# Optimization experiments

Hardware: AMD Instinct MI355X
Metric: run time of the kernel (lower is better)

## Reference

```python
import jax, jax.numpy as jnp
import numpy as np

S = 8        # parallel streams (encoder/decoder pairs)
T_ENC = 12   # encoder timesteps per stream
H = 256      # hidden size
F = 316      # input features
B = 1024     # batch
MAX_LEN = 48
SCALE = 1.0 / np.sqrt(H).astype(np.float32)  # MHA single-head scaling


def _lstm_gates_to_hc(gates, c):
    # PyTorch gate order: i, f, g, o
    i, f, g, o = jnp.split(gates, 4, axis=-1)
    c_new = jax.nn.sigmoid(f) * c + jax.nn.sigmoid(i) * jnp.tanh(g)
    h_new = jax.nn.sigmoid(o) * jnp.tanh(c_new)
    return h_new, c_new


def setup_inputs() -> dict:
    key = jax.random.key(0)
    ks = jax.random.split(key, 20)
    w = 0.05
    inp = {
        'x': jax.random.normal(ks[0], (B, 96, F), jnp.float32),
        'tgt': jax.random.normal(ks[1], (B, MAX_LEN), jnp.float32),
        # encoder LSTM (per-stream stacked): input F -> H
        'W_ih_e': jax.random.normal(ks[2], (S, 4 * H, F), jnp.float32) * w,
        'W_hh_e': jax.random.normal(ks[3], (S, 4 * H, H), jnp.float32) * w,
        'b_ih_e': jnp.zeros((S, 4 * H), jnp.float32),
        'b_hh_e': jnp.zeros((S, 4 * H), jnp.float32),
        # decoder LSTM: input 1 -> H
        'W_ih_d': jax.random.normal(ks[4], (S, 4 * H, 1), jnp.float32) * w,
        'W_hh_d': jax.random.normal(ks[5], (S, 4 * H, H), jnp.float32) * w,
        'b_ih_d': jnp.zeros((S, 4 * H), jnp.float32),
        'b_hh_d': jnp.zeros((S, 4 * H), jnp.float32),
        # MultiheadAttention: in_proj [3H,H] per stream, out_proj [H,H]
        'W_in_attn': jax.random.normal(ks[6], (S, 3 * H, H), jnp.float32) * w,
        'b_in_attn': jnp.zeros((S, 3 * H), jnp.float32),
        'W_out_attn': jax.random.normal(ks[7], (S, H, H), jnp.float32) * w,
        'b_out_attn': jnp.zeros((S, H), jnp.float32),
        # decoder out_fc: 2H -> 1
        'W_fcout': jax.random.normal(ks[8], (S, 1, 2 * H), jnp.float32) * w,
        'b_fcout': jnp.zeros((S, 1), jnp.float32),
        # final fc: 8 -> 1
        'W_fc': jax.random.normal(ks[9], (1, S), jnp.float32) * w,
        'b_fc': jnp.zeros((1,), jnp.float32),
    }
    return inp


def _forward(x, tgt, W_ih_e, W_hh_e, b_ih_e, b_hh_e,
             W_ih_d, W_hh_d, b_ih_d, b_hh_d,
             W_in_attn, b_in_attn, W_out_attn, b_out_attn,
             W_fcout, b_fcout, W_fc, b_fc):
    batch, max_len = x.shape[0], tgt.shape[1]
    # time-major then split 96 steps into 8 streams of 12: [S, T_ENC, B, F]
    xe = x.transpose(1, 0, 2).reshape(S, T_ENC, batch, F)

    # ---- encoders: batched LSTM over 8 streams ----
    def enc_step(carry, xt):  # xt [S,B,F]
        h, c = carry
        gates = (jnp.einsum('sbf,sgf->sbg', xt, W_ih_e) + b_ih_e[:, None, :]
                 + jnp.einsum('sbh,sgh->sbg', h, W_hh_e) + b_hh_e[:, None, :])
        h, c = _lstm_gates_to_hc(gates, c)
        return (h, c), h

    h0 = jnp.zeros((S, batch, H), x.dtype)
    (hT, cT), enc_out = jax.lax.scan(enc_step, (h0, h0), xe.transpose(1, 0, 2, 3))
    # enc_out: [T_ENC, S, B, H]; (hT, cT) seed the decoder hidden state

    # ---- precompute attention K,V ----
    Wq, Wk, Wv = jnp.split(W_in_attn, 3, axis=1)  # each [S,H,H]
    bq, bk, bv = jnp.split(b_in_attn, 3, axis=1)  # each [S,H]
    k = jnp.einsum('tsbh,seh->tsbe', enc_out, Wk) + bk[None, :, None, :]
    v = jnp.einsum('tsbh,seh->tsbe', enc_out, Wv) + bv[None, :, None, :]

    # teacher-forced decoder inputs: step 0 uses x[-1,:,0], step t uses tgt[:,t-1]
    inputs = jnp.concatenate([x[:, -1, 0][None, :], tgt.T[:-1]], axis=0)  # [L,B]

    def dec_step(carry, inp):  # inp [B]
        h, c = carry
        it = jnp.broadcast_to(inp[None, :, None], (S, h.shape[1], 1))
        gates = (jnp.einsum('sbi,sgi->sbg', it, W_ih_d) + b_ih_d[:, None, :]
                 + jnp.einsum('sbh,sgh->sbg', h, W_hh_d) + b_hh_d[:, None, :])
        h, c = _lstm_gates_to_hc(gates, c)
        # single-query MHA (1 head) against encoder outputs
        q = jnp.einsum('sbh,seh->sbe', h, Wq) + bq[:, None, :]
        scores = jnp.einsum('sbe,tsbe->sbt', q, k) * SCALE
        attn = jax.nn.softmax(scores, axis=-1)
        ctx = jnp.einsum('sbt,tsbe->sbe', attn, v)
        ctx = jnp.einsum('sbe,soe->sbo', ctx, W_out_attn) + b_out_attn[:, None, :]
        cat = jnp.concatenate([h, ctx], axis=-1)  # [S,B,2H]
        out = jnp.einsum('sbk,sok->sbo', cat, W_fcout) + b_fcout[:, None, :]
        return (h, c), out[..., 0]  # [S,B]

    _, outs = jax.lax.scan(dec_step, (hT, cT), inputs)  # [L,S,B]
    final = outs.transpose(0, 2, 1)                      # [L,B,S]
    y = jnp.einsum('lbs,os->lbo', final, W_fc) + b_fc    # [L,B,1]
    return y[..., 0].T                                    # [B,L]


def reference(x, tgt, W_ih_e, W_hh_e, b_ih_e, b_hh_e,
              W_ih_d, W_hh_d, b_ih_d, b_hh_d,
              W_in_attn, b_in_attn, W_out_attn, b_out_attn,
              W_fcout, b_fcout, W_fc, b_fc):
    return _forward(x, tgt, W_ih_e, W_hh_e, b_ih_e, b_hh_e,
                    W_ih_d, W_hh_d, b_ih_d, b_hh_d,
                    W_in_attn, b_in_attn, W_out_attn, b_out_attn,
                    W_fcout, b_fcout, W_fc, b_fc)
```

## Files before the change

kernel.cpp:

```cpp
#include <hip/hip_runtime.h>
#include <cstdio>
#include <cstdint>

#define S8     8
#define TENC   12
#define HDIM   256
#define FDIM   316
#define BATCH  1024
#define LDEC   48
#define DBT    32
#define KA     264
#define SCALE_ATTN 0.0625f

typedef short bf16x8 __attribute__((ext_vector_type(8)));
typedef float f32x4  __attribute__((ext_vector_type(4)));

__device__ __forceinline__ float sigf(float x) { return 1.0f / (1.0f + expf(-x)); }

__device__ __forceinline__ unsigned short f2bf(float f) {
  unsigned u = __builtin_bit_cast(unsigned, f);
  unsigned r = (u + 0x7fffu + ((u >> 16) & 1u)) >> 16;
  return (unsigned short)r;
}
__device__ __forceinline__ float bflo(unsigned u) {
  return __builtin_bit_cast(float, u << 16);
}
__device__ __forceinline__ float bfhi(unsigned u) {
  return __builtin_bit_cast(float, u & 0xffff0000u);
}

#define MFMA(acc, a, b) acc = __builtin_amdgcn_mfma_f32_16x16x32_bf16(a, b, acc, 0, 0, 0)

#define DOT8(a, q, hp) \
  a = fmaf(bflo(q.x), hp[0], a); a = fmaf(bfhi(q.x), hp[1], a); \
  a = fmaf(bflo(q.y), hp[2], a); a = fmaf(bfhi(q.y), hp[3], a); \
  a = fmaf(bflo(q.z), hp[4], a); a = fmaf(bfhi(q.z), hp[5], a); \
  a = fmaf(bflo(q.w), hp[6], a); a = fmaf(bfhi(q.w), hp[7], a);

#define UNPS(dst, off, q) \
  dst[off+0] = bflo(q.x); dst[off+1] = bfhi(q.x); \
  dst[off+2] = bflo(q.y); dst[off+3] = bfhi(q.y); \
  dst[off+4] = bflo(q.z); dst[off+5] = bfhi(q.z); \
  dst[off+6] = bflo(q.w); dst[off+7] = bfhi(q.w);

__global__ __launch_bounds__(256) void transpose_k(const float* __restrict__ in,
                                                   float* __restrict__ out,
                                                   int R, int C) {
  __shared__ float tile[32][33];
  const int s = blockIdx.z;
  const size_t base = (size_t)s * R * C;
  const int r0 = blockIdx.y * 32, c0 = blockIdx.x * 32;
  const int tx = threadIdx.x & 31, ty = threadIdx.x >> 5;
  for (int i = ty; i < 32; i += 8) {
    int r = r0 + i, c = c0 + tx;
    if (r < R && c < C) tile[i][tx] = in[base + (size_t)r * C + c];
  }
  __syncthreads();
  for (int i = ty; i < 32; i += 8) {
    int c = c0 + i, r = r0 + tx;
    if (c < C && r < R) out[base + (size_t)c * R + r] = tile[tx][i];
  }
}

__global__ __launch_bounds__(256) void fold_gemm(const float* __restrict__ A, size_t sA,
                                                 const float* __restrict__ Bm, size_t sB,
                                                 float* __restrict__ out, size_t sO) {
  const int s = blockIdx.y, r0 = blockIdx.x * 32, col = threadIdx.x;
  A += (size_t)s * sA; Bm += (size_t)s * sB; out += (size_t)s * sO;
  float acc[32] = {};
  for (int e = 0; e < HDIM; ++e) {
    const float bvv = Bm[(size_t)e * HDIM + col];
#pragma unroll
    for (int r = 0; r < 32; ++r) acc[r] = fmaf(A[(size_t)e * HDIM + r0 + r], bvv, acc[r]);
  }
  for (int r = 0; r < 32; ++r) out[(size_t)(r0 + r) * HDIM + col] = acc[r];
}

__global__ __launch_bounds__(64) void pack_hl(const float* __restrict__ src, int Ksrc, int ksT,
                                              bf16x8* __restrict__ outhi,
                                              bf16x8* __restrict__ outlo) {
  const int s = blockIdx.z, ks = blockIdx.y, nt = blockIdx.x;
  const int lane = threadIdx.x, l15 = lane & 15, quad = lane >> 4;
  const int n = nt * 16 + l15, kb = ks * 32 + quad * 8;
  const float* row = src + ((size_t)s * 1024 + n) * Ksrc;
  union { bf16x8 v; unsigned short e[8]; } h, l;
#pragma unroll
  for (int j = 0; j < 8; ++j) {
    const int k = kb + j;
    const float v = (k < Ksrc) ? row[k] : 0.f;
    const unsigned short hi = f2bf(v);
    h.e[j] = hi;
    l.e[j] = f2bf(v - bflo(hi));
  }
  const size_t idx = (((size_t)s * ksT + ks) * 64 + nt) * 64 + lane;
  outhi[idx] = h.v;
  outlo[idx] = l.v;
}

__global__ __launch_bounds__(64) void pack_s(const float* __restrict__ src, int ntOff,
                                             bf16x8* __restrict__ out) {
  const int s = blockIdx.z, ks = blockIdx.y, nt = blockIdx.x;
  const int lane = threadIdx.x, l15 = lane & 15, quad = lane >> 4;
  const int n = nt * 16 + l15, kb = ks * 32 + quad * 8;
  const float* row = src + ((size_t)s * 256 + n) * 256;
  union { bf16x8 v; unsigned short e[8]; } h;
#pragma unroll
  for (int j = 0; j < 8; ++j) h.e[j] = f2bf(row[kb + j]);
  out[(((size_t)s * 8 + ks) * 32 + ntOff + nt) * 64 + lane] = h.v;
}

__global__ __launch_bounds__(256) void fold_vec2(const float* __restrict__ Win,
                                                 const float* __restrict__ bin,
                                                 const float* __restrict__ Wout,
                                                 const float* __restrict__ bout,
                                                 float* __restrict__ kbv,
                                                 float* __restrict__ cbias) {
  const int s = blockIdx.x, t = threadIdx.x;
  const float* bq = bin + s * 768;
  const float* bv = bin + s * 768 + 512;
  float a0 = 0.f, a1 = 0.f;
  for (int e = 0; e < 256; ++e) {
    a0 = fmaf(Win[((size_t)s * 768 + 256 + e) * 256 + t], bq[e], a0);
    a1 = fmaf(Wout[((size_t)s * 256 + t) * 256 + e], bv[e], a1);
  }
  kbv[s * 256 + t] = a0;
  cbias[s * 256 + t] = a1 + bout[s * 256 + t];
}

__global__ __launch_bounds__(256) void fold_mvw(const float* __restrict__ Mv,
                                                const float* __restrict__ Wfo,
                                                float* __restrict__ mvw) {
  const int s = blockIdx.x, k = threadIdx.x;
  float a = 0.f;
  for (int o = 0; o < 256; ++o)
    a = fmaf(Wfo[s * 512 + 256 + o], Mv[((size_t)s * 256 + o) * 256 + k], a);
  mvw[s * 256 + k] = a;
}

__global__ void fold_bias(const float* __restrict__ a, const float* __restrict__ b,
                          float* __restrict__ o, int n) {
  int i = blockIdx.x * 256 + threadIdx.x;
  if (i < n) o[i] = a[i] + b[i];
}

__global__ void build_decin(const float* __restrict__ x, const float* __restrict__ tgt,
                            float* __restrict__ dec_in) {
  int idx = blockIdx.x * 256 + threadIdx.x;
  if (idx >= LDEC * BATCH) return;
  int l = idx >> 10, b = idx & 1023;
  dec_in[idx] = (l == 0) ? x[(size_t)b * 96 * FDIM + 95 * FDIM]
                         : tgt[(size_t)b * LDEC + (l - 1)];
}

__global__ __launch_bounds__(512) void rec_phase(
    const float* __restrict__ x,
    const bf16x8* __restrict__ WxH, const bf16x8* __restrict__ WxL,
    const bf16x8* __restrict__ WeH, const bf16x8* __restrict__ WeL,
    const bf16x8* __restrict__ WdH, const bf16x8* __restrict__ WdL,
    const float* __restrict__ be, const float* __restrict__ bd,
    const float* __restrict__ wihd, const float* __restrict__ Wfo,
    const float* __restrict__ decin,
    unsigned* __restrict__ hEnc,
    unsigned short* __restrict__ hDec,
    float* __restrict__ hdPart)
{
  __shared__ unsigned short hAhi[DBT * KA];
  __shared__ unsigned short hAlo[DBT * KA];
  __shared__ float scrR[DBT * 8];

  const int bid = blockIdx.x;
  const int s = bid & 7, b0 = (bid >> 3) * DBT;
  const int tid = threadIdx.x;
  const int w = tid >> 6, lane = tid & 63, l15 = lane & 15, quad = lane >> 4;

  for (int i = tid; i < DBT * KA; i += 512) { hAhi[i] = 0; hAlo[i] = 0; }

  float beV[4][2], bdV[4][2], wdV[4][2], wfoV[2];
#pragma unroll
  for (int g = 0; g < 4; ++g)
#pragma unroll
    for (int st = 0; st < 2; ++st) {
      const int J = g * 256 + 32 * w + 16 * st + l15;
      beV[g][st] = be[s * 1024 + J];
      bdV[g][st] = bd[s * 1024 + J];
      wdV[g][st] = wihd[s * 1024 + J];
    }
#pragma unroll
  for (int st = 0; st < 2; ++st) wfoV[st] = Wfo[s * 512 + 32 * w + 16 * st + l15];

  float cst[2][2][4];
#pragma unroll
  for (int a = 0; a < 2; ++a)
#pragma unroll
    for (int b = 0; b < 2; ++b)
#pragma unroll
      for (int r = 0; r < 4; ++r) cst[a][b][r] = 0.f;

  const bf16x8* wxh = WxH + (size_t)s * 10 * 64 * 64;
  const bf16x8* wxl = WxL + (size_t)s * 10 * 64 * 64;
  const bf16x8* weh = WeH + (size_t)s * 8 * 64 * 64;
  const bf16x8* wel = WeL + (size_t)s * 8 * 64 * 64;
  const bf16x8* wdh = WdH + (size_t)s * 8 * 64 * 64;
  const bf16x8* wdl = WdL + (size_t)s * 8 * 64 * 64;

  __syncthreads();

  for (int t = 0; t < TENC; ++t) {
    f32x4 acc[2][2][4];
#pragma unroll
    for (int mt = 0; mt < 2; ++mt)
#pragma unroll
      for (int st = 0; st < 2; ++st)
#pragma unroll
        for (int c = 0; c < 4; ++c) acc[mt][st][c] = (f32x4){0.f, 0.f, 0.f, 0.f};

    const size_t xoff = (size_t)(s * TENC + t) * FDIM;
    for (int ks = 0; ks < 10; ++ks) {
      bf16x8 axh[2], axl[2];
#pragma unroll
      for (int mt = 0; mt < 2; ++mt) {
        const f32x4* xr = (const f32x4*)(x + (size_t)(b0 + 16 * mt + l15) * (96 * FDIM)
                                         + xoff + ks * 32 + quad * 8);
        const f32x4 v0 = __builtin_nontemporal_load(xr);
        f32x4 v1;
        if (ks == 9 && quad == 3) v1 = (f32x4){0.f, 0.f, 0.f, 0.f};
        else v1 = __builtin_nontemporal_load(xr + 1);
        float vv[8];
#pragma unroll
        for (int j = 0; j < 4; ++j) { vv[j] = v0[j]; vv[4 + j] = v1[j]; }
        union { bf16x8 v; unsigned short e[8]; } uh, ul;
#pragma unroll
        for (int j = 0; j < 8; ++j) {
          const unsigned short hi = f2bf(vv[j]);
          uh.e[j] = hi;
          ul.e[j] = f2bf(vv[j] - bflo(hi));
        }
        axh[mt] = uh.v; axl[mt] = ul.v;
      }
#pragma unroll
      for (int st = 0; st < 2; ++st)
#pragma unroll
        for (int c = 0; c < 4; ++c) {
          const int nt = c * 16 + 2 * w + st;
          const bf16x8 bh = wxh[(ks * 64 + nt) * 64 + lane];
          const bf16x8 bl = wxl[(ks * 64 + nt) * 64 + lane];
          MFMA(acc[0][st][c], axh[0], bh); MFMA(acc[0][st][c], axh[0], bl); MFMA(acc[0][st][c], axl[0], bh);
          MFMA(acc[1][st][c], axh[1], bh); MFMA(acc[1][st][c], axh[1], bl); MFMA(acc[1][st][c], axl[1], bh);
        }
    }
#pragma unroll 2
    for (int ks = 0; ks < 8; ++ks) {
      bf16x8 ah[2], al[2];
#pragma unroll
      for (int mt = 0; mt < 2; ++mt) {
        const int ao = (16 * mt + l15) * KA + ks * 32 + quad * 8;
        ah[mt] = *(const bf16x8*)&hAhi[ao];
        al[mt] = *(const bf16x8*)&hAlo[ao];
      }
#pragma unroll
      for (int st = 0; st < 2; ++st)
#pragma unroll
        for (int c = 0; c < 4; ++c) {
          const int nt = c * 16 + 2 * w + st;
          const bf16x8 bh = weh[(ks * 64 + nt) * 64 + lane];
          const bf16x8 bl = wel[(ks * 64 + nt) * 64 + lane];
          MFMA(acc[0][st][c], ah[0], bh); MFMA(acc[0][st][c], ah[0], bl); MFMA(acc[0][st][c], al[0], bh);
          MFMA(acc[1][st][c], ah[1], bh); MFMA(acc[1][st][c], ah[1], bl); MFMA(acc[1][st][c], al[1], bh);
        }
    }
    float hv[2][2][4];
#pragma unroll
    for (int mt = 0; mt < 2; ++mt)
#pragma unroll
      for (int st = 0; st < 2; ++st)
#pragma unroll
        for (int reg = 0; reg < 4; ++reg) {
          const float gi = sigf(acc[mt][st][0][reg] + beV[0][st]);
          const float gf = sigf(acc[mt][st][1][reg] + beV[1][st]);
          const float gg = tanhf(acc[mt][st][2][reg] + beV[2][st]);
          const float go = sigf(acc[mt][st][3][reg] + beV[3][st]);
          const float cn = fmaf(gf, cst[mt][st][reg], gi * gg);
          cst[mt][st][reg] = cn;
          hv[mt][st][reg] = go * tanhf(cn);
        }
    __syncthreads();
#pragma unroll
    for (int mt = 0; mt < 2; ++mt)
#pragma unroll
      for (int st = 0; st < 2; ++st)
#pragma unroll
        for (int reg = 0; reg < 4; ++reg) {
          const int R = 16 * mt + 4 * quad + reg;
          const int J = 32 * w + 16 * st + l15;
          const float v = hv[mt][st][reg];
          const unsigned short hi = f2bf(v);
          const unsigned short lo = f2bf(v - bflo(hi));
          hAhi[R * KA + J] = hi;
          hAlo[R * KA + J] = lo;
          __builtin_nontemporal_store((unsigned)hi | ((unsigned)lo << 16),
              &hEnc[((size_t)(t * S8 + s) * BATCH + b0 + R) * HDIM + J]);
        }
    __syncthreads();
  }

  for (int l = 0; l < LDEC; ++l) {
    f32x4 acc[2][2][4];
#pragma unroll
    for (int mt = 0; mt < 2; ++mt)
#pragma unroll
      for (int st = 0; st < 2; ++st)
#pragma unroll
        for (int c = 0; c < 4; ++c) acc[mt][st][c] = (f32x4){0.f, 0.f, 0.f, 0.f};

#pragma unroll 2
    for (int ks = 0; ks < 8; ++ks) {
      bf16x8 ah[2], al[2];
#pragma unroll
      for (int mt = 0; mt < 2; ++mt) {
        const int ao = (16 * mt + l15) * KA + ks * 32 + quad * 8;
        ah[mt] = *(const bf16x8*)&hAhi[ao];
        al[mt] = *(const bf16x8*)&hAlo[ao];
      }
#pragma unroll
      for (int st = 0; st < 2; ++st)
#pragma unroll
        for (int c = 0; c < 4; ++c) {
          const int nt = c * 16 + 2 * w + st;
          const bf16x8 bh = wdh[(ks * 64 + nt) * 64 + lane];
          const bf16x8 bl = wdl[(ks * 64 + nt) * 64 + lane];
          MFMA(acc[0][st][c], ah[0], bh); MFMA(acc[0][st][c], ah[0], bl); MFMA(acc[0][st][c], al[0], bh);
          MFMA(acc[1][st][c], ah[1], bh); MFMA(acc[1][st][c], ah[1], bl); MFMA(acc[1][st][c], al[1], bh);
        }
    }
    float hv[2][2][4];
#pragma unroll
    for (int mt = 0; mt < 2; ++mt)
#pragma unroll
      for (int reg = 0; reg < 4; ++reg) {
        const int R = 16 * mt + 4 * quad + reg;
        const float it = decin[(size_t)l * BATCH + b0 + R];
#pragma unroll
        for (int st = 0; st < 2; ++st) {
          const float gi = sigf(fmaf(it, wdV[0][st], acc[mt][st][0][reg] + bdV[0][st]));
          const float gf = sigf(fmaf(it, wdV[1][st], acc[mt][st][1][reg] + bdV[1][st]));
          const float gg = tanhf(fmaf(it, wdV[2][st], acc[mt][st][2][reg] + bdV[2][st]));
          const float go = sigf(fmaf(it, wdV[3][st], acc[mt][st][3][reg] + bdV[3][st]));
          const float cn = fmaf(gf, cst[mt][st][reg], gi * gg);
          cst[mt][st][reg] = cn;
          hv[mt][st][reg] = go * tanhf(cn);
        }
      }
    __syncthreads();
#pragma unroll
    for (int mt = 0; mt < 2; ++mt)
#pragma unroll
      for (int st = 0; st < 2; ++st)
#pragma unroll
        for (int reg = 0; reg < 4; ++reg) {
          const int R = 16 * mt + 4 * quad + reg;
          const int J = 32 * w + 16 * st + l15;
          const float v = hv[mt][st][reg];
          const unsigned short hi = f2bf(v);
          hAhi[R * KA + J] = hi;
          hAlo[R * KA + J] = f2bf(v - bflo(hi));
          __builtin_nontemporal_store(hi,
              &hDec[((size_t)(l * S8 + s) * BATCH + b0 + R) * HDIM + J]);
        }
    {
      float part[8];
#pragma unroll
      for (int mt = 0; mt < 2; ++mt)
#pragma unroll
        for (int reg = 0; reg < 4; ++reg)
          part[mt * 4 + reg] = hv[mt][0][reg] * wfoV[0] + hv[mt][1][reg] * wfoV[1];
#pragma unroll
      for (int i = 0; i < 8; ++i) {
        float v = part[i];
        v += __shfl_xor(v, 1, 16);
        v += __shfl_xor(v, 2, 16);
        v += __shfl_xor(v, 4, 16);
        v += __shfl_xor(v, 8, 16);
        part[i] = v;
      }
      if (l15 == 0) {
#pragma unroll
        for (int mt = 0; mt < 2; ++mt)
#pragma unroll
          for (int reg = 0; reg < 4; ++reg)
            scrR[(16 * mt + 4 * quad + reg) * 8 + w] = part[mt * 4 + reg];
      }
    }
    __syncthreads();
    if (tid < DBT) {
      float a = 0.f;
#pragma unroll
      for (int p = 0; p < 8; ++p) a += scrR[tid * 8 + p];
      hdPart[((size_t)l * S8 + s) * BATCH + b0 + tid] = a;
    }
  }
}

__global__ __launch_bounds__(256) void attn_phase(
    const unsigned* __restrict__ hEnc, const unsigned short* __restrict__ hDec,
    const bf16x8* __restrict__ AMvF,
    const float* __restrict__ kbv, const float* __restrict__ cbias,
    const float* __restrict__ mvw,
    const float* __restrict__ Wfo, const float* __restrict__ bfo,
    const float* __restrict__ hdPart,
    float* __restrict__ douts)
{
  __shared__ unsigned short kpL[TENC][16][KA];
  __shared__ float scr[16 * TENC * 17];
  __shared__ float sc[16][TENC];
  __shared__ float kbs[TENC][16];
  __shared__ float vw[TENC][16];

  const int s = blockIdx.y, b0 = blockIdx.x * 16;
  const int tid = threadIdx.x;
  const int w = tid >> 6, lane = tid & 63, l15 = lane & 15, quad = lane >> 4;

  const bf16x8* amv = AMvF + (size_t)s * 8 * 32 * 64;
  const float* kvv = kbv + s * 256;
  const float* mvv = mvw + s * 256;
  const float* cbs = cbias + s * 256;
  const float* wfo = Wfo + s * 512;
  const float bfos = bfo[s];

  float cw = 0.f;
  for (int e = 0; e < 256; ++e) cw = fmaf(cbs[e], wfo[256 + e], cw);

  for (int t = 0; t < TENC; ++t) {
    f32x4 acc[4];
#pragma unroll
    for (int c = 0; c < 4; ++c) acc[c] = (f32x4){0.f, 0.f, 0.f, 0.f};
    for (int ks = 0; ks < 8; ++ks) {
      const unsigned* hp = hEnc + ((size_t)(t * S8 + s) * BATCH + b0 + l15) * HDIM
                         + ks * 32 + quad * 8;
      union { bf16x8 v; unsigned short e[8]; } uh, ul;
#pragma unroll
      for (int j = 0; j < 8; ++j) {
        const unsigned u = hp[j];
        uh.e[j] = (unsigned short)u;
        ul.e[j] = (unsigned short)(u >> 16);
      }
#pragma unroll
      for (int c = 0; c < 4; ++c) {
        const int nt = w * 4 + c;
        const bf16x8 b = amv[(ks * 32 + nt) * 64 + lane];
        MFMA(acc[c], uh.v, b); MFMA(acc[c], ul.v, b);
// ... 84 lines not shown
#pragma unroll
  for (int s = 0; s < S8; ++s)
    a = fmaf(douts[((size_t)l * S8 + s) * BATCH + b], Wfc[s], a);
  out[idx] = a;
}

extern "C" void kernel_launch(void* const* d_in, const int* in_sizes, int n_in,
                              void* d_out, int out_size, void* d_ws, size_t ws_size,
                              hipStream_t stream) {
  const float* x          = (const float*)d_in[0];
  const float* tgt        = (const float*)d_in[1];
  const float* W_ih_e     = (const float*)d_in[2];
  const float* W_hh_e     = (const float*)d_in[3];
  const float* b_ih_e     = (const float*)d_in[4];
  const float* b_hh_e     = (const float*)d_in[5];
  const float* W_ih_d     = (const float*)d_in[6];
  const float* W_hh_d     = (const float*)d_in[7];
  const float* b_ih_d     = (const float*)d_in[8];
  const float* b_hh_d     = (const float*)d_in[9];
  const float* W_in_attn  = (const float*)d_in[10];
  const float* b_in_attn  = (const float*)d_in[11];
  const float* W_out_attn = (const float*)d_in[12];
  const float* b_out_attn = (const float*)d_in[13];
  const float* W_fcout    = (const float*)d_in[14];
  const float* b_fcout    = (const float*)d_in[15];
  const float* W_fc       = (const float*)d_in[16];
  const float* b_fc       = (const float*)d_in[17];

  char* wsb = (char*)d_ws;
  size_t off = 0;
  auto alloc = [&](size_t bytes) {
    void* p = wsb + off; off += (bytes + 255) & ~(size_t)255; return p;
  };
  float*  douts = (float*)alloc((size_t)LDEC * S8 * BATCH * 4);
  float*  decin = (float*)alloc((size_t)LDEC * BATCH * 4);
  float*  hdPart= (float*)alloc((size_t)LDEC * S8 * BATCH * 4);
  float*  Pmat  = (float*)alloc((size_t)S8 * 256 * 256 * 4);
  float*  Mvmat = (float*)alloc((size_t)S8 * 256 * 256 * 4);
  float*  WoT   = (float*)alloc((size_t)S8 * 256 * 256 * 4);
  bf16x8* WxH   = (bf16x8*)alloc((size_t)S8 * 10 * 64 * 64 * 16);
  bf16x8* WxL   = (bf16x8*)alloc((size_t)S8 * 10 * 64 * 64 * 16);
  bf16x8* WeH   = (bf16x8*)alloc((size_t)S8 * 8 * 64 * 64 * 16);
  bf16x8* WeL   = (bf16x8*)alloc((size_t)S8 * 8 * 64 * 64 * 16);
  bf16x8* WdH   = (bf16x8*)alloc((size_t)S8 * 8 * 64 * 64 * 16);
  bf16x8* WdL   = (bf16x8*)alloc((size_t)S8 * 8 * 64 * 64 * 16);
  bf16x8* AMvF  = (bf16x8*)alloc((size_t)S8 * 8 * 32 * 64 * 16);
  float*  kbv   = (float*)alloc((size_t)S8 * 256 * 4);
  float*  cbias = (float*)alloc((size_t)S8 * 256 * 4);
  float*  mvw   = (float*)alloc((size_t)S8 * 256 * 4);
  float*  beF   = (float*)alloc((size_t)S8 * 1024 * 4);
  float*  bdF   = (float*)alloc((size_t)S8 * 1024 * 4);
  unsigned* hEnc = (unsigned*)alloc((size_t)TENC * S8 * BATCH * HDIM * 4);
  unsigned short* hDec = (unsigned short*)alloc((size_t)LDEC * S8 * BATCH * HDIM * 2);
  if (off > ws_size) {
    fprintf(stderr, "kernel_launch: ws too small: need %zu bytes, have %zu\n", off, ws_size);
    return;
  }

  transpose_k<<<dim3(8, 8, S8), 256, 0, stream>>>(W_out_attn, WoT, 256, 256);
  fold_gemm<<<dim3(8, S8), 256, 0, stream>>>(W_in_attn, (size_t)768 * 256,
                                             W_in_attn + 256 * 256, (size_t)768 * 256,
                                             Pmat, (size_t)256 * 256);
  fold_gemm<<<dim3(8, S8), 256, 0, stream>>>(WoT, (size_t)256 * 256,
                                             W_in_attn + 2 * 256 * 256, (size_t)768 * 256,
                                             Mvmat, (size_t)256 * 256);
  pack_hl<<<dim3(64, 10, S8), 64, 0, stream>>>(W_ih_e, FDIM, 10, WxH, WxL);
  pack_hl<<<dim3(64, 8, S8), 64, 0, stream>>>(W_hh_e, 256, 8, WeH, WeL);
  pack_hl<<<dim3(64, 8, S8), 64, 0, stream>>>(W_hh_d, 256, 8, WdH, WdL);
  pack_s<<<dim3(16, 8, S8), 64, 0, stream>>>(Pmat, 0, AMvF);
  fold_vec2<<<S8, 256, 0, stream>>>(W_in_attn, b_in_attn, W_out_attn, b_out_attn, kbv, cbias);
  fold_mvw<<<S8, 256, 0, stream>>>(Mvmat, W_fcout, mvw);
  fold_bias<<<(S8 * 1024 + 255) / 256, 256, 0, stream>>>(b_ih_e, b_hh_e, beF, S8 * 1024);
  fold_bias<<<(S8 * 1024 + 255) / 256, 256, 0, stream>>>(b_ih_d, b_hh_d, bdF, S8 * 1024);
  build_decin<<<(LDEC * BATCH + 255) / 256, 256, 0, stream>>>(x, tgt, decin);

  rec_phase<<<256, 512, 0, stream>>>(
      x, WxH, WxL, WeH, WeL, WdH, WdL, beF, bdF, W_ih_d, W_fcout, decin,
      hEnc, hDec, hdPart);

  attn_phase<<<dim3(64, S8), 256, 0, stream>>>(
      hEnc, hDec, AMvF, kbv, cbias, mvw, W_fcout, b_fcout, hdPart, douts);

  final_fc<<<(BATCH * LDEC + 255) / 256, 256, 0, stream>>>(douts, W_fc, b_fc, (float*)d_out);
}
```

Before: 3.228 ms.

## Halve recurrent batch tile to 16 rows and use 512 blocks of 4 waves

```diff
diff --git a/kernel.cpp b/kernel.cpp
--- a/kernel.cpp
+++ b/kernel.cpp
@@ -8,7 +8,7 @@
 #define FDIM   316
 #define BATCH  1024
 #define LDEC   48
-#define DBT    32
+#define DBT    16
 #define KA     264
 #define SCALE_ATTN 0.0625f
 
@@ -152,7 +152,7 @@
                          : tgt[(size_t)b * LDEC + (l - 1)];
 }
 
-__global__ __launch_bounds__(512) void rec_phase(
+__global__ __launch_bounds__(256) void rec_phase(
     const float* __restrict__ x,
     const bf16x8* __restrict__ WxH, const bf16x8* __restrict__ WxL,
     const bf16x8* __restrict__ WeH, const bf16x8* __restrict__ WeL,
@@ -166,35 +166,33 @@
 {
   __shared__ unsigned short hAhi[DBT * KA];
   __shared__ unsigned short hAlo[DBT * KA];
-  __shared__ float scrR[DBT * 8];
+  __shared__ float scrR[DBT * 4];
 
   const int bid = blockIdx.x;
   const int s = bid & 7, b0 = (bid >> 3) * DBT;
   const int tid = threadIdx.x;
   const int w = tid >> 6, lane = tid & 63, l15 = lane & 15, quad = lane >> 4;
 
-  for (int i = tid; i < DBT * KA; i += 512) { hAhi[i] = 0; hAlo[i] = 0; }
-
-  float beV[4][2], bdV[4][2], wdV[4][2], wfoV[2];
+  for (int i = tid; i < DBT * KA; i += 256) { hAhi[i] = 0; hAlo[i] = 0; }
+
+  float beV[4][4], bdV[4][4], wdV[4][4], wfoV[4];
 #pragma unroll
   for (int g = 0; g < 4; ++g)
 #pragma unroll
-    for (int st = 0; st < 2; ++st) {
-      const int J = g * 256 + 32 * w + 16 * st + l15;
+    for (int st = 0; st < 4; ++st) {
+      const int J = g * 256 + 64 * w + 16 * st + l15;
       beV[g][st] = be[s * 1024 + J];
       bdV[g][st] = bd[s * 1024 + J];
       wdV[g][st] = wihd[s * 1024 + J];
     }
 #pragma unroll
-  for (int st = 0; st < 2; ++st) wfoV[st] = Wfo[s * 512 + 32 * w + 16 * st + l15];
-
-  float cst[2][2][4];
-#pragma unroll
-  for (int a = 0; a < 2; ++a)
-#pragma unroll
-    for (int b = 0; b < 2; ++b)
-#pragma unroll
-      for (int r = 0; r < 4; ++r) cst[a][b][r] = 0.f;
+  for (int st = 0; st < 4; ++st) wfoV[st] = Wfo[s * 512 + 64 * w + 16 * st + l15];
+
+  float cst[4][4];
+#pragma unroll
+  for (int a = 0; a < 4; ++a)
+#pragma unroll
+    for (int r = 0; r < 4; ++r) cst[a][r] = 0.f;
 
   const bf16x8* wxh = WxH + (size_t)s * 10 * 64 * 64;
   const bf16x8* wxl = WxL + (size_t)s * 10 * 64 * 64;
@@ -206,20 +204,17 @@
   __syncthreads();
 
   for (int t = 0; t < TENC; ++t) {
-    f32x4 acc[2][2][4];
-#pragma unroll
-    for (int mt = 0; mt < 2; ++mt)
-#pragma unroll
-      for (int st = 0; st < 2; ++st)
-#pragma unroll
-        for (int c = 0; c < 4; ++c) acc[mt][st][c] = (f32x4){0.f, 0.f, 0.f, 0.f};
+    f32x4 acc[4][4];
+#pragma unroll
+    for (int g = 0; g < 4; ++g)
+#pragma unroll
+      for (int st = 0; st < 4; ++st) acc[g][st] = (f32x4){0.f, 0.f, 0.f, 0.f};
 
     const size_t xoff = (size_t)(s * TENC + t) * FDIM;
     for (int ks = 0; ks < 10; ++ks) {
-      bf16x8 axh[2], axl[2];
-#pragma unroll
-      for (int mt = 0; mt < 2; ++mt) {
-        const f32x4* xr = (const f32x4*)(x + (size_t)(b0 + 16 * mt + l15) * (96 * FDIM)
+      bf16x8 axh, axl;
+      {
+        const f32x4* xr = (const f32x4*)(x + (size_t)(b0 + l15) * (96 * FDIM)
                                          + xoff + ks * 32 + quad * 8);
         const f32x4 v0 = __builtin_nontemporal_load(xr);
         f32x4 v1;
@@ -235,146 +230,132 @@
           uh.e[j] = hi;
           ul.e[j] = f2bf(vv[j] - bflo(hi));
         }
-        axh[mt] = uh.v; axl[mt] = ul.v;
-      }
-#pragma unroll
-      for (int st = 0; st < 2; ++st)
-#pragma unroll
-        for (int c = 0; c < 4; ++c) {
-          const int nt = c * 16 + 2 * w + st;
+        axh = uh.v; axl = ul.v;
+      }
+#pragma unroll
+      for (int g = 0; g < 4; ++g)
+#pragma unroll
+        for (int st = 0; st < 4; ++st) {
+          const int nt = g * 16 + 4 * w + st;
           const bf16x8 bh = wxh[(ks * 64 + nt) * 64 + lane];
           const bf16x8 bl = wxl[(ks * 64 + nt) * 64 + lane];
-          MFMA(acc[0][st][c], axh[0], bh); MFMA(acc[0][st][c], axh[0], bl); MFMA(acc[0][st][c], axl[0], bh);
-          MFMA(acc[1][st][c], axh[1], bh); MFMA(acc[1][st][c], axh[1], bl); MFMA(acc[1][st][c], axl[1], bh);
+          MFMA(acc[g][st], axh, bh); MFMA(acc[g][st], axh, bl); MFMA(acc[g][st], axl, bh);
         }
     }
 #pragma unroll 2
     for (int ks = 0; ks < 8; ++ks) {
-      bf16x8 ah[2], al[2];
-#pragma unroll
-      for (int mt = 0; mt < 2; ++mt) {
-        const int ao = (16 * mt + l15) * KA + ks * 32 + quad * 8;
-        ah[mt] = *(const bf16x8*)&hAhi[ao];
-        al[mt] = *(const bf16x8*)&hAlo[ao];
-      }
-#pragma unroll
-      for (int st = 0; st < 2; ++st)
-#pragma unroll
-        for (int c = 0; c < 4; ++c) {
-          const int nt = c * 16 + 2 * w + st;
+      const int ao = l15 * KA + ks * 32 + quad * 8;
+      const bf16x8 ah = *(const bf16x8*)&hAhi[ao];
+      const bf16x8 al = *(const bf16x8*)&hAlo[ao];
+#pragma unroll
+      for (int g = 0; g < 4; ++g)
+#pragma unroll
+        for (int st = 0; st < 4; ++st) {
+          const int nt = g * 16 + 4 * w + st;
           const bf16x8 bh = weh[(ks * 64 + nt) * 64 + lane];
           const bf16x8 bl = wel[(ks * 64 + nt) * 64 + lane];
-          MFMA(acc[0][st][c], ah[0], bh); MFMA(acc[0][st][c], ah[0], bl); MFMA(acc[0][st][c], al[0], bh);
-          MFMA(acc[1][st][c], ah[1], bh); MFMA(acc[1][st][c], ah[1], bl); MFMA(acc[1][st][c], al[1], bh);
+          MFMA(acc[g][st], ah, bh); MFMA(acc[g][st], ah, bl); MFMA(acc[g][st], al, bh);
         }
     }
-    float hv[2][2][4];
-#pragma unroll
-    for (int mt = 0; mt < 2; ++mt)
-#pragma unroll
-      for (int st = 0; st < 2; ++st)
-#pragma unroll
-        for (int reg = 0; reg < 4; ++reg) {
-          const float gi = sigf(acc[mt][st][0][reg] + beV[0][st]);
-          const float gf = sigf(acc[mt][st][1][reg] + beV[1][st]);
-          const float gg = tanhf(acc[mt][st][2][reg] + beV[2][st]);
-          const float go = sigf(acc[mt][st][3][reg] + beV[3][st]);
-          const float cn = fmaf(gf, cst[mt][st][reg], gi * gg);
-          cst[mt][st][reg] = cn;
-          hv[mt][st][reg] = go * tanhf(cn);
-        }
-    __syncthreads();
-#pragma unroll
-    for (int mt = 0; mt < 2; ++mt)
-#pragma unroll
-      for (int st = 0; st < 2; ++st)
-#pragma unroll
-        for (int reg = 0; reg < 4; ++reg) {
-          const int R = 16 * mt + 4 * quad + reg;
-          const int J = 32 * w + 16 * st + l15;
-          const float v = hv[mt][st][reg];
-          const unsigned short hi = f2bf(v);
-          const unsigned short lo = f2bf(v - bflo(hi));
-          hAhi[R * KA + J] = hi;
-          hAlo[R * KA + J] = lo;
-          __builtin_nontemporal_store((unsigned)hi | ((unsigned)lo << 16),
-              &hEnc[((size_t)(t * S8 + s) * BATCH + b0 + R) * HDIM + J]);
-        }
+    float hv[4][4];
+#pragma unroll
+    for (int st = 0; st < 4; ++st)
+#pragma unroll
+      for (int reg = 0; reg < 4; ++reg) {
+        const float gi = sigf(acc[0][st][reg] + beV[0][st]);
+        const float gf = sigf(acc[1][st][reg] + beV[1][st]);
+        const float gg = tanhf(acc[2][st][reg] + beV[2][st]);
+        const float go = sigf(acc[3][st][reg] + beV[3][st]);
+        const float cn = fmaf(gf, cst[st][reg], gi * gg);
+        cst[st][reg] = cn;
+        hv[st][reg] = go * tanhf(cn);
+      }
+    __syncthreads();
+#pragma unroll
+    for (int st = 0; st < 4; ++st)
+#pragma unroll
+      for (int reg = 0; reg < 4; ++reg) {
+        const int R = 4 * quad + reg;
+        const int J = 64 * w + 16 * st + l15;
+        const float v = hv[st][reg];
+        const unsigned short hi = f2bf(v);
+        const unsigned short lo = f2bf(v - bflo(hi));
+        hAhi[R * KA + J] = hi;
+        hAlo[R * KA + J] = lo;
+        __builtin_nontemporal_store((unsigned)hi | ((unsigned)lo << 16),
+            &hEnc[((size_t)(t * S8 + s) * BATCH + b0 + R) * HDIM + J]);
+      }
     __syncthreads();
   }
 
   for (int l = 0; l < LDEC; ++l) {
-    f32x4 acc[2][2][4];
-#pragma unroll
-    for (int mt = 0; mt < 2; ++mt)
-#pragma unroll
-      for (int st = 0; st < 2; ++st)
-#pragma unroll
-        for (int c = 0; c < 4; ++c) acc[mt][st][c] = (f32x4){0.f, 0.f, 0.f, 0.f};
+    f32x4 acc[4][4];
+#pragma unroll
+    for (int g = 0; g < 4; ++g)
+#pragma unroll
+      for (int st = 0; st < 4; ++st) acc[g][st] = (f32x4){0.f, 0.f, 0.f, 0.f};
 
 #pragma unroll 2
     for (int ks = 0; ks < 8; ++ks) {
-      bf16x8 ah[2], al[2];
-#pragma unroll
-      for (int mt = 0; mt < 2; ++mt) {
-        const int ao = (16 * mt + l15) * KA + ks * 32 + quad * 8;
-        ah[mt] = *(const bf16x8*)&hAhi[ao];
-        al[mt] = *(const bf16x8*)&hAlo[ao];
-      }
-#pragma unroll
-      for (int st = 0; st < 2; ++st)
-#pragma unroll
-        for (int c = 0; c < 4; ++c) {
-          const int nt = c * 16 + 2 * w + st;
+      const int ao = l15 * KA + ks * 32 + quad * 8;
+      const bf16x8 ah = *(const bf16x8*)&hAhi[ao];
+      const bf16x8 al = *(const bf16x8*)&hAlo[ao];
+#pragma unroll
+      for (int g = 0; g < 4; ++g)
+#pragma unroll
+        for (int st = 0; st < 4; ++st) {
+          const int nt = g * 16 + 4 * w + st;
           const bf16x8 bh = wdh[(ks * 64 + nt) * 64 + lane];
           const bf16x8 bl = wdl[(ks * 64 + nt) * 64 + lane];
-          MFMA(acc[0][st][c], ah[0], bh); MFMA(acc[0][st][c], ah[0], bl); MFMA(acc[0][st][c], al[0], bh);
-          MFMA(acc[1][st][c], ah[1], bh); MFMA(acc[1][st][c], ah[1], bl); MFMA(acc[1][st][c], al[1], bh);
+          MFMA(acc[g][st], ah, bh); MFMA(acc[g][st], ah, bl); MFMA(acc[g][st], al, bh);
         }
     }
-    float hv[2][2][4];
-#pragma unroll
-    for (int mt = 0; mt < 2; ++mt)
+    float hv[4][4];
+    {
+      float itv[4];
+#pragma unroll
+      for (int reg = 0; reg < 4; ++reg)
+        itv[reg] = decin[(size_t)l * BATCH + b0 + 4 * quad + reg];
 #pragma unroll
       for (int reg = 0; reg < 4; ++reg) {
-        const int R = 16 * mt + 4 * quad + reg;
-        const float it = decin[(size_t)l * BATCH + b0 + R];
-#pragma unroll
-        for (int st = 0; st < 2; ++st) {
-          const float gi = sigf(fmaf(it, wdV[0][st], acc[mt][st][0][reg] + bdV[0][st]));
-          const float gf = sigf(fmaf(it, wdV[1][st], acc[mt][st][1][reg] + bdV[1][st]));
-          const float gg = tanhf(fmaf(it, wdV[2][st], acc[mt][st][2][reg] + bdV[2][st]));
-          const float go = sigf(fmaf(it, wdV[3][st], acc[mt][st][3][reg] + bdV[3][st]));
-          const float cn = fmaf(gf, cst[mt][st][reg], gi * gg);
-          cst[mt][st][reg] = cn;
-          hv[mt][st][reg] = go * tanhf(cn);
+        const float it = itv[reg];
+#pragma unroll
+        for (int st = 0; st < 4; ++st) {
+          const float gi = sigf(fmaf(it, wdV[0][st], acc[0][st][reg] + bdV[0][st]));
+          const float gf = sigf(fmaf(it, wdV[1][st], acc[1][st][reg] + bdV[1][st]));
+          const float gg = tanhf(fmaf(it, wdV[2][st], acc[2][st][reg] + bdV[2][st]));
+          const float go = sigf(fmaf(it, wdV[3][st], acc[3][st][reg] + bdV[3][st]));
+          const float cn = fmaf(gf, cst[st][reg], gi * gg);
+          cst[st][reg] = cn;
+          hv[st][reg] = go * tanhf(cn);
         }
       }
-    __syncthreads();
-#pragma unroll
-    for (int mt = 0; mt < 2; ++mt)
-#pragma unroll
-      for (int st = 0; st < 2; ++st)
-#pragma unroll
-        for (int reg = 0; reg < 4; ++reg) {
-          const int R = 16 * mt + 4 * quad + reg;
-          const int J = 32 * w + 16 * st + l15;
-          const float v = hv[mt][st][reg];
-          const unsigned short hi = f2bf(v);
-          hAhi[R * KA + J] = hi;
-          hAlo[R * KA + J] = f2bf(v - bflo(hi));
-          __builtin_nontemporal_store(hi,
-              &hDec[((size_t)(l * S8 + s) * BATCH + b0 + R) * HDIM + J]);
-        }
+    }
+    __syncthreads();
+#pragma unroll
+    for (int st = 0; st < 4; ++st)
+#pragma unroll
+      for (int reg = 0; reg < 4; ++reg) {
+        const int R = 4 * quad + reg;
+        const int J = 64 * w + 16 * st + l15;
+        const float v = hv[st][reg];
+        const unsigned short hi = f2bf(v);
+        hAhi[R * KA + J] = hi;
+        hAlo[R * KA + J] = f2bf(v - bflo(hi));
+        __builtin_nontemporal_store(hi,
+            &hDec[((size_t)(l * S8 + s) * BATCH + b0 + R) * HDIM + J]);
+      }
     {
-      float part[8];
-#pragma unroll
-      for (int mt = 0; mt < 2; ++mt)
-#pragma unroll
-        for (int reg = 0; reg < 4; ++reg)
-          part[mt * 4 + reg] = hv[mt][0][reg] * wfoV[0] + hv[mt][1][reg] * wfoV[1];
-#pragma unroll
-      for (int i = 0; i < 8; ++i) {
+      float part[4];
+#pragma unroll
+      for (int reg = 0; reg < 4; ++reg) {
+        float a = 0.f;
+#pragma unroll
+        for (int st = 0; st < 4; ++st) a = fmaf(hv[st][reg], wfoV[st], a);
+        part[reg] = a;
+      }
+#pragma unroll
+      for (int i = 0; i < 4; ++i) {
         float v = part[i];
         v += __shfl_xor(v, 1, 16);
         v += __shfl_xor(v, 2, 16);
@@ -384,17 +365,15 @@
       }
       if (l15 == 0) {
 #pragma unroll
-        for (int mt = 0; mt < 2; ++mt)
-#pragma unroll
-          for (int reg = 0; reg < 4; ++reg)
-            scrR[(16 * mt + 4 * quad + reg) * 8 + w] = part[mt * 4 + reg];
+        for (int reg = 0; reg < 4; ++reg)
+          scrR[(4 * quad + reg) * 4 + w] = part[reg];
       }
     }
     __syncthreads();
     if (tid < DBT) {
       float a = 0.f;
 #pragma unroll
-      for (int p = 0; p < 8; ++p) a += scrR[tid * 8 + p];
+      for (int p = 0; p < 4; ++p) a += scrR[tid * 4 + p];
       hdPart[((size_t)l * S8 + s) * BATCH + b0 + tid] = a;
     }
   }
@@ -607,7 +586,7 @@
   fold_bias<<<(S8 * 1024 + 255) / 256, 256, 0, stream>>>(b_ih_d, b_hh_d, bdF, S8 * 1024);
   build_decin<<<(LDEC * BATCH + 255) / 256, 256, 0, stream>>>(x, tgt, decin);
 
-  rec_phase<<<256, 512, 0, stream>>>(
+  rec_phase<<<512, 256, 0, stream>>>(
       x, WxH, WxL, WeH, WeL, WdH, WdL, beF, bdF, W_ih_d, W_fcout, decin,
       hEnc, hDec, hdPart);
 
```

Measured after the change: 3.946 ms. 1.22x slower.

## Double rec_phase threads to 1024 and pre-pack x into bf16 hi/lo

Applied to the files above, without the earlier changes.

```diff
diff --git a/kernel.cpp b/kernel.cpp
--- a/kernel.cpp
+++ b/kernel.cpp
@@ -6,6 +6,7 @@
 #define TENC   12
 #define HDIM   256
 #define FDIM   316
+#define FPAD   320
 #define BATCH  1024
 #define LDEC   48
 #define DBT    32
@@ -74,6 +75,20 @@
     for (int r = 0; r < 32; ++r) acc[r] = fmaf(A[(size_t)e * HDIM + r0 + r], bvv, acc[r]);
   }
   for (int r = 0; r < 32; ++r) out[(size_t)(r0 + r) * HDIM + col] = acc[r];
+}
+
+__global__ void pack_x(const float* __restrict__ x,
+                       unsigned short* __restrict__ xH,
+                       unsigned short* __restrict__ xL) {
+  const size_t idx = (size_t)blockIdx.x * 256 + threadIdx.x;
+  if (idx >= (size_t)BATCH * 96 * FPAD) return;
+  const int k = (int)(idx % FPAD);
+  const size_t bt = idx / FPAD;
+  float v = 0.f;
+  if (k < FDIM) v = x[bt * FDIM + k];
+  const unsigned short hi = f2bf(v);
+  xH[idx] = hi;
+  xL[idx] = f2bf(v - bflo(hi));
 }
 
 __global__ __launch_bounds__(64) void pack_hl(const float* __restrict__ src, int Ksrc, int ksT,
@@ -152,8 +167,8 @@
                          : tgt[(size_t)b * LDEC + (l - 1)];
 }
 
-__global__ __launch_bounds__(512) void rec_phase(
-    const float* __restrict__ x,
+__global__ __launch_bounds__(1024) void rec_phase(
+    const unsigned short* __restrict__ xH, const unsigned short* __restrict__ xL,
     const bf16x8* __restrict__ WxH, const bf16x8* __restrict__ WxL,
     const bf16x8* __restrict__ WeH, const bf16x8* __restrict__ WeL,
     const bf16x8* __restrict__ WdH, const bf16x8* __restrict__ WdL,
@@ -166,35 +181,31 @@
 {
   __shared__ unsigned short hAhi[DBT * KA];
   __shared__ unsigned short hAlo[DBT * KA];
-  __shared__ float scrR[DBT * 8];
+  __shared__ float beS[1024];
+  __shared__ float bdS[1024];
+  __shared__ float wdS[1024];
+  __shared__ float wfoS[256];
+  __shared__ float scrR[DBT * 16];
 
   const int bid = blockIdx.x;
   const int s = bid & 7, b0 = (bid >> 3) * DBT;
   const int tid = threadIdx.x;
   const int w = tid >> 6, lane = tid & 63, l15 = lane & 15, quad = lane >> 4;
-
-  for (int i = tid; i < DBT * KA; i += 512) { hAhi[i] = 0; hAlo[i] = 0; }
-
-  float beV[4][2], bdV[4][2], wdV[4][2], wfoV[2];
-#pragma unroll
-  for (int g = 0; g < 4; ++g)
-#pragma unroll
-    for (int st = 0; st < 2; ++st) {
-      const int J = g * 256 + 32 * w + 16 * st + l15;
-      beV[g][st] = be[s * 1024 + J];
-      bdV[g][st] = bd[s * 1024 + J];
-      wdV[g][st] = wihd[s * 1024 + J];
-    }
-#pragma unroll
-  for (int st = 0; st < 2; ++st) wfoV[st] = Wfo[s * 512 + 32 * w + 16 * st + l15];
-
-  float cst[2][2][4];
+  const int JJ = 16 * w + l15;
+
+  for (int i = tid; i < DBT * KA; i += 1024) { hAhi[i] = 0; hAlo[i] = 0; }
+  if (tid < 1024) {
+    beS[tid] = be[s * 1024 + tid];
+    bdS[tid] = bd[s * 1024 + tid];
+    wdS[tid] = wihd[s * 1024 + tid];
+  }
+  if (tid < 256) wfoS[tid] = Wfo[s * 512 + tid];
+
+  float cst[2][4];
 #pragma unroll
   for (int a = 0; a < 2; ++a)
 #pragma unroll
-    for (int b = 0; b < 2; ++b)
-#pragma unroll
-      for (int r = 0; r < 4; ++r) cst[a][b][r] = 0.f;
+    for (int r = 0; r < 4; ++r) cst[a][r] = 0.f;
 
   const bf16x8* wxh = WxH + (size_t)s * 10 * 64 * 64;
   const bf16x8* wxl = WxL + (size_t)s * 10 * 64 * 64;
@@ -206,49 +217,31 @@
   __syncthreads();
 
   for (int t = 0; t < TENC; ++t) {
-    f32x4 acc[2][2][4];
+    f32x4 acc[2][4];
 #pragma unroll
     for (int mt = 0; mt < 2; ++mt)
 #pragma unroll
-      for (int st = 0; st < 2; ++st)
-#pragma unroll
-        for (int c = 0; c < 4; ++c) acc[mt][st][c] = (f32x4){0.f, 0.f, 0.f, 0.f};
-
-    const size_t xoff = (size_t)(s * TENC + t) * FDIM;
+      for (int g = 0; g < 4; ++g) acc[mt][g] = (f32x4){0.f, 0.f, 0.f, 0.f};
+
+    const size_t xoff = (size_t)(s * TENC + t) * FPAD;
     for (int ks = 0; ks < 10; ++ks) {
       bf16x8 axh[2], axl[2];
 #pragma unroll
       for (int mt = 0; mt < 2; ++mt) {
-        const f32x4* xr = (const f32x4*)(x + (size_t)(b0 + 16 * mt + l15) * (96 * FDIM)
-                                         + xoff + ks * 32 + quad * 8);
-        const f32x4 v0 = __builtin_nontemporal_load(xr);
-        f32x4 v1;
-        if (ks == 9 && quad == 3) v1 = (f32x4){0.f, 0.f, 0.f, 0.f};
-        else v1 = __builtin_nontemporal_load(xr + 1);
-        float vv[8];
-#pragma unroll
-        for (int j = 0; j < 4; ++j) { vv[j] = v0[j]; vv[4 + j] = v1[j]; }
-        union { bf16x8 v; unsigned short e[8]; } uh, ul;
-#pragma unroll
-        for (int j = 0; j < 8; ++j) {
-          const unsigned short hi = f2bf(vv[j]);
-          uh.e[j] = hi;
-          ul.e[j] = f2bf(vv[j] - bflo(hi));
-        }
-        axh[mt] = uh.v; axl[mt] = ul.v;
-      }
-#pragma unroll
-      for (int st = 0; st < 2; ++st)
-#pragma unroll
-        for (int c = 0; c < 4; ++c) {
-          const int nt = c * 16 + 2 * w + st;
-          const bf16x8 bh = wxh[(ks * 64 + nt) * 64 + lane];
-          const bf16x8 bl = wxl[(ks * 64 + nt) * 64 + lane];
-          MFMA(acc[0][st][c], axh[0], bh); MFMA(acc[0][st][c], axh[0], bl); MFMA(acc[0][st][c], axl[0], bh);
-          MFMA(acc[1][st][c], axh[1], bh); MFMA(acc[1][st][c], axh[1], bl); MFMA(acc[1][st][c], axl[1], bh);
-        }
-    }
-#pragma unroll 2
+        const size_t ro = (size_t)(b0 + 16 * mt + l15) * (96 * FPAD) + xoff
+                        + ks * 32 + quad * 8;
+        axh[mt] = *(const bf16x8*)&xH[ro];
+        axl[mt] = *(const bf16x8*)&xL[ro];
+      }
+#pragma unroll
+      for (int g = 0; g < 4; ++g) {
+        const int nt = g * 16 + w;
+        const bf16x8 bh = wxh[(ks * 64 + nt) * 64 + lane];
+        const bf16x8 bl = wxl[(ks * 64 + nt) * 64 + lane];
+        MFMA(acc[0][g], axh[0], bh); MFMA(acc[0][g], axh[0], bl); MFMA(acc[0][g], axl[0], bh);
+        MFMA(acc[1][g], axh[1], bh); MFMA(acc[1][g], axh[1], bl); MFMA(acc[1][g], axl[1], bh);
+      }
+    }
     for (int ks = 0; ks < 8; ++ks) {
       bf16x8 ah[2], al[2];
 #pragma unroll
@@ -258,61 +251,57 @@
         al[mt] = *(const bf16x8*)&hAlo[ao];
       }
 #pragma unroll
-      for (int st = 0; st < 2; ++st)
-#pragma unroll
-        for (int c = 0; c < 4; ++c) {
-          const int nt = c * 16 + 2 * w + st;
-          const bf16x8 bh = weh[(ks * 64 + nt) * 64 + lane];
-          const bf16x8 bl = wel[(ks * 64 + nt) * 64 + lane];
-          MFMA(acc[0][st][c], ah[0], bh); MFMA(acc[0][st][c], ah[0], bl); MFMA(acc[0][st][c], al[0], bh);
-          MFMA(acc[1][st][c], ah[1], bh); MFMA(acc[1][st][c], ah[1], bl); MFMA(acc[1][st][c], al[1], bh);
+      for (int g = 0; g < 4; ++g) {
+        const int nt = g * 16 + w;
+        const bf16x8 bh = weh[(ks * 64 + nt) * 64 + lane];
+        const bf16x8 bl = wel[(ks * 64 + nt) * 64 + lane];
+        MFMA(acc[0][g], ah[0], bh); MFMA(acc[0][g], ah[0], bl); MFMA(acc[0][g], al[0], bh);
+        MFMA(acc[1][g], ah[1], bh); MFMA(acc[1][g], ah[1], bl); MFMA(acc[1][g], al[1], bh);
+      }
+    }
+    float hv[2][4];
+    {
+      const float g0 = beS[JJ];
+      const float g1 = beS[256 + JJ];
+      const float g2 = beS[512 + JJ];
+      const float g3 = beS[768 + JJ];
+#pragma unroll
+      for (int mt = 0; mt < 2; ++mt)
+#pragma unroll
+        for (int reg = 0; reg < 4; ++reg) {
+          const float gi = sigf(acc[mt][0][reg] + g0);
+          const float gf = sigf(acc[mt][1][reg] + g1);
+          const float gg = tanhf(acc[mt][2][reg] + g2);
+          const float go = sigf(acc[mt][3][reg] + g3);
+          const float cn = fmaf(gf, cst[mt][reg], gi * gg);
+          cst[mt][reg] = cn;
+          hv[mt][reg] = go * tanhf(cn);
         }
     }
-    float hv[2][2][4];
+    __syncthreads();
 #pragma unroll
     for (int mt = 0; mt < 2; ++mt)
 #pragma unroll
-      for (int st = 0; st < 2; ++st)
-#pragma unroll
-        for (int reg = 0; reg < 4; ++reg) {
-          const float gi = sigf(acc[mt][st][0][reg] + beV[0][st]);
-          const float gf = sigf(acc[mt][st][1][reg] + beV[1][st]);
-          const float gg = tanhf(acc[mt][st][2][reg] + beV[2][st]);
-          const float go = sigf(acc[mt][st][3][reg] + beV[3][st]);
-          const float cn = fmaf(gf, cst[mt][st][reg], gi * gg);
-          cst[mt][st][reg] = cn;
-          hv[mt][st][reg] = go * tanhf(cn);
-        }
-    __syncthreads();
+      for (int reg = 0; reg < 4; ++reg) {
+        const int R = 16 * mt + 4 * quad + reg;
+        const float v = hv[mt][reg];
+        const unsigned short hi = f2bf(v);
+        const unsigned short lo = f2bf(v - bflo(hi));
+        hAhi[R * KA + JJ] = hi;
+        hAlo[R * KA + JJ] = lo;
+        __builtin_nontemporal_store((unsigned)hi | ((unsigned)lo << 16),
+            &hEnc[((size_t)(t * S8 + s) * BATCH + b0 + R) * HDIM + JJ]);
+      }
+    __syncthreads();
+  }
+
+  for (int l = 0; l < LDEC; ++l) {
+    f32x4 acc[2][4];
 #pragma unroll
     for (int mt = 0; mt < 2; ++mt)
 #pragma unroll
-      for (int st = 0; st < 2; ++st)
-#pragma unroll
-        for (int reg = 0; reg < 4; ++reg) {
-          const int R = 16 * mt + 4 * quad + reg;
-          const int J = 32 * w + 16 * st + l15;
-          const float v = hv[mt][st][reg];
-          const unsigned short hi = f2bf(v);
-          const unsigned short lo = f2bf(v - bflo(hi));
-          hAhi[R * KA + J] = hi;
-          hAlo[R * KA + J] = lo;
-          __builtin_nontemporal_store((unsigned)hi | ((unsigned)lo << 16),
-              &hEnc[((size_t)(t * S8 + s) * BATCH + b0 + R) * HDIM + J]);
-        }
-    __syncthreads();
-  }
-
-  for (int l = 0; l < LDEC; ++l) {
-    f32x4 acc[2][2][4];
-#pragma unroll
-    for (int mt = 0; mt < 2; ++mt)
-#pragma unroll
-      for (int st = 0; st < 2; ++st)
-#pragma unroll
-        for (int c = 0; c < 4; ++c) acc[mt][st][c] = (f32x4){0.f, 0.f, 0.f, 0.f};
-
-#pragma unroll 2
+      for (int g = 0; g < 4; ++g) acc[mt][g] = (f32x4){0.f, 0.f, 0.f, 0.f};
+
     for (int ks = 0; ks < 8; ++ks) {
       bf16x8 ah[2], al[2];
 #pragma unroll
@@ -322,57 +311,59 @@
         al[mt] = *(const bf16x8*)&hAlo[ao];
       }
 #pragma unroll
-      for (int st = 0; st < 2; ++st)
-#pragma unroll
-        for (int c = 0; c < 4; ++c) {
-          const int nt = c * 16 + 2 * w + st;
-          const bf16x8 bh = wdh[(ks * 64 + nt) * 64 + lane];
-          const bf16x8 bl = wdl[(ks * 64 + nt) * 64 + lane];
-          MFMA(acc[0][st][c], ah[0], bh); MFMA(acc[0][st][c], ah[0], bl); MFMA(acc[0][st][c], al[0], bh);
-          MFMA(acc[1][st][c], ah[1], bh); MFMA(acc[1][st][c], ah[1], bl); MFMA(acc[1][st][c], al[1], bh);
+      for (int g = 0; g < 4; ++g) {
+        const int nt = g * 16 + w;
+        const bf16x8 bh = wdh[(ks * 64 + nt) * 64 + lane];
+        const bf16x8 bl = wdl[(ks * 64 + nt) * 64 + lane];
+        MFMA(acc[0][g], ah[0], bh); MFMA(acc[0][g], ah[0], bl); MFMA(acc[0][g], al[0], bh);
+        MFMA(acc[1][g], ah[1], bh); MFMA(acc[1][g], ah[1], bl); MFMA(acc[1][g], al[1], bh);
+      }
+    }
+    float hv[2][4];
+    {
+      const float b0g = bdS[JJ];
+      const float b1g = bdS[256 + JJ];
+      const float b2g = bdS[512 + JJ];
+      const float b3g = bdS[768 + JJ];
+      const float w0g = wdS[JJ];
+      const float w1g = wdS[256 + JJ];
+      const float w2g = wdS[512 + JJ];
+      const float w3g = wdS[768 + JJ];
+#pragma unroll
+      for (int mt = 0; mt < 2; ++mt)
+#pragma unroll
+        for (int reg = 0; reg < 4; ++reg) {
+          const int R = 16 * mt + 4 * quad + reg;
+          const float it = decin[(size_t)l * BATCH + b0 + R];
+          const float gi = sigf(fmaf(it, w0g, acc[mt][0][reg] + b0g));
+          const float gf = sigf(fmaf(it, w1g, acc[mt][1][reg] + b1g));
+          const float gg = tanhf(fmaf(it, w2g, acc[mt][2][reg] + b2g));
+          const float go = sigf(fmaf(it, w3g, acc[mt][3][reg] + b3g));
+          const float cn = fmaf(gf, cst[mt][reg], gi * gg);
+          cst[mt][reg] = cn;
+          hv[mt][reg] = go * tanhf(cn);
         }
     }
-    float hv[2][2][4];
+    __syncthreads();
 #pragma unroll
     for (int mt = 0; mt < 2; ++mt)
 #pragma unroll
       for (int reg = 0; reg < 4; ++reg) {
         const int R = 16 * mt + 4 * quad + reg;
-        const float it = decin[(size_t)l * BATCH + b0 + R];
-#pragma unroll
-        for (int st = 0; st < 2; ++st) {
-          const float gi = sigf(fmaf(it, wdV[0][st], acc[mt][st][0][reg] + bdV[0][st]));
-          const float gf = sigf(fmaf(it, wdV[1][st], acc[mt][st][1][reg] + bdV[1][st]));
-          const float gg = tanhf(fmaf(it, wdV[2][st], acc[mt][st][2][reg] + bdV[2][st]));
-          const float go = sigf(fmaf(it, wdV[3][st], acc[mt][st][3][reg] + bdV[3][st]));
-          const float cn = fmaf(gf, cst[mt][st][reg], gi * gg);
-          cst[mt][st][reg] = cn;
-          hv[mt][st][reg] = go * tanhf(cn);
-        }
-      }
-    __syncthreads();
-#pragma unroll
-    for (int mt = 0; mt < 2; ++mt)
-#pragma unroll
-      for (int st = 0; st < 2; ++st)
-#pragma unroll
-        for (int reg = 0; reg < 4; ++reg) {
-          const int R = 16 * mt + 4 * quad + reg;
-          const int J = 32 * w + 16 * st + l15;
-          const float v = hv[mt][st][reg];
-          const unsigned short hi = f2bf(v);
-          hAhi[R * KA + J] = hi;
-          hAlo[R * KA + J] = f2bf(v - bflo(hi));
-          __builtin_nontemporal_store(hi,
-              &hDec[((size_t)(l * S8 + s) * BATCH + b0 + R) * HDIM + J]);
-        }
+        const float v = hv[mt][reg];
+        const unsigned short hi = f2bf(v);
+        hAhi[R * KA + JJ] = hi;
+        hAlo[R * KA + JJ] = f2bf(v - bflo(hi));
+        __builtin_nontemporal_store(hi,
+            &hDec[((size_t)(l * S8 + s) * BATCH + b0 + R) * HDIM + JJ]);
+      }
     {
       float part[8];
 #pragma unroll
       for (int mt = 0; mt < 2; ++mt)
 #pragma unroll
         for (int reg = 0; reg < 4; ++reg)
-          part[mt * 4 + reg] = hv[mt][0][reg] * wfoV[0] + hv[mt][1][reg] * wfoV[1];
+          part[mt * 4 + reg] = hv[mt][reg] * wfoS[JJ];
 #pragma unroll
       for (int i = 0; i < 8; ++i) {
         float v = part[i];
@@ -387,14 +378,14 @@
         for (int mt = 0; mt < 2; ++mt)
 #pragma unroll
           for (int reg = 0; reg < 4; ++reg)
-            scrR[(16 * mt + 4 * quad + reg) * 8 + w] = part[mt * 4 + reg];
+            scrR[(16 * mt + 4 * quad + reg) * 16 + w] = part[mt * 4 + reg];
       }
     }
     __syncthreads();
     if (tid < DBT) {
       float a = 0.f;
 #pragma unroll
-      for (int p = 0; p < 8; ++p) a += scrR[tid * 8 + p];
+      for (int p = 0; p < 16; ++p) a += scrR[tid * 16 + p];
       hdPart[((size_t)l * S8 + s) * BATCH + b0 + tid] = a;
     }
   }
@@ -585,6 +576,8 @@
   float*  bdF   = (float*)alloc((size_t)S8 * 1024 * 4);
   unsigned* hEnc = (unsigned*)alloc((size_t)TENC * S8 * BATCH * HDIM * 4);
   unsigned short* hDec = (unsigned short*)alloc((size_t)LDEC * S8 * BATCH * HDIM * 2);
+  unsigned short* xHb = (unsigned short*)alloc((size_t)BATCH * 96 * FPAD * 2);
+  unsigned short* xLb = (unsigned short*)alloc((size_t)BATCH * 96 * FPAD * 2);
   if (off > ws_size) {
     fprintf(stderr, "kernel_launch: ws too small: need %zu bytes, have %zu\n", off, ws_size);
     return;
@@ -597,6 +590,7 @@
   fold_gemm<<<dim3(8, S8), 256, 0, stream>>>(WoT, (size_t)256 * 256,
                                              W_in_attn + 2 * 256 * 256, (size_t)768 * 256,
                                              Mvmat, (size_t)256 * 256);
+  pack_x<<<(int)(((size_t)BATCH * 96 * FPAD + 255) / 256), 256, 0, stream>>>(x, xHb, xLb);
   pack_hl<<<dim3(64, 10, S8), 64, 0, stream>>>(W_ih_e, FDIM, 10, WxH, WxL);
   pack_hl<<<dim3(64, 8, S8), 64, 0, stream>>>(W_hh_e, 256, 8, WeH, WeL);
   pack_hl<<<dim3(64, 8, S8), 64, 0, stream>>>(W_hh_d, 256, 8, WdH, WdL);
@@ -607,8 +601,8 @@
   fold_bias<<<(S8 * 1024 + 255) / 256, 256, 0, stream>>>(b_ih_d, b_hh_d, bdF, S8 * 1024);
   build_decin<<<(LDEC * BATCH + 255) / 256, 256, 0, stream>>>(x, tgt, decin);
 
-  rec_phase<<<256, 512, 0, stream>>>(
-      x, WxH, WxL, WeH, WeL, WdH, WdL, beF, bdF, W_ih_d, W_fcout, decin,
+  rec_phase<<<256, 1024, 0, stream>>>(
+      xHb, xLb, WxH, WxL, WeH, WeL, WdH, WdL, beF, bdF, W_ih_d, W_fcout, decin,
       hEnc, hDec, hdPart);
 
   attn_phase<<<dim3(64, S8), 256, 0, stream>>>(
```

After: 4.580 ms. 41.9% more time.
